# Performance work log

Hardware: AMD Instinct MI355X
Metric: run time of the kernel (lower is better)

## Reference

```python
import jax, jax.numpy as jnp
import numpy as np

H = 512  # hidden_size
A = 1.0  # hard_sigm slope


def hard_sigm(a, x):
    return jnp.clip((a * x + 1.0) / 2.0, 0.0, 1.0)


def setup_inputs() -> dict:
    key = jax.random.key(0)
    ks = jax.random.split(key, 10)
    B = 8192
    bottom, top = 512, 512
    stdv = 1.0 / np.sqrt(H)
    u = lambda k, shp: jax.random.uniform(k, shp, jnp.float32, -stdv, stdv)
    return {
        "c": jax.random.normal(ks[0], (H, B), jnp.float32),
        "h_bottom": jax.random.normal(ks[1], (bottom, B), jnp.float32),
        "h": jax.random.normal(ks[2], (H, B), jnp.float32),
        "h_top": jax.random.normal(ks[3], (top, B), jnp.float32),
        "z": jax.random.uniform(ks[4], (1, B), jnp.float32),
        "z_bottom": jax.random.uniform(ks[5], (1, B), jnp.float32),
        "U_11": u(ks[6], (4 * H + 1, H)),
        "U_21": u(ks[7], (4 * H + 1, top)),
        "W_01": u(ks[8], (4 * H + 1, bottom)),
        "bias": u(ks[9], (4 * H + 1,)),
    }


def reference(c, h_bottom, h, h_top, z, z_bottom, U_11, U_21, W_01, bias):
    # z, z_bottom: (1, B) boundary indicators broadcast over the gate axis
    s_recur = (1.0 - z) * (U_11 @ h)          # (4H+1, B)
    s_topdown = z * (U_21 @ h_top)            # last_layer=False
    s_bottomup = z_bottom * (W_01 @ h_bottom)
    f_s = s_recur + s_topdown + s_bottomup + bias[:, None]

    f = jax.nn.sigmoid(f_s[0:H, :])
    i = jax.nn.sigmoid(f_s[H:2 * H, :])
    o = jax.nn.sigmoid(f_s[2 * H:3 * H, :])
    g = jnp.tanh(f_s[3 * H:4 * H, :])
    z_hat = hard_sigm(A, f_s[4 * H:4 * H + 1, :])  # (1, B)

    ig = i * g
    c_new = z * ig + (1.0 - z) * (1.0 - z_bottom) * c \
        + (1.0 - z) * z_bottom * (f * c + ig)
    tanh_c = jnp.tanh(c_new)
    h_new = z * o * tanh_c + (1.0 - z) * (1.0 - z_bottom) * h \
        + (1.0 - z) * z_bottom * o * tanh_c
    return (h_new, c_new, z_hat)
```

## Files before the change

kernel.cpp:

```cpp
#include <hip/hip_runtime.h>
#include <hip/hip_bf16.h>

#define HH 512
#define BB 8192
#define KK 1536
#define NT 48
#define HB 4194304
#define BLOB 8192

typedef __bf16 bhalf;
typedef __bf16 bf16x8 __attribute__((ext_vector_type(8)));
typedef float  f32x4  __attribute__((ext_vector_type(4)));

typedef __attribute__((address_space(1))) void* as1_t;
typedef __attribute__((address_space(3))) void* as3_t;

#define GLDS(src, dst) __builtin_amdgcn_global_load_lds((as1_t)(void*)(src), (as3_t)(void*)(dst), 16, 0, 0)
#define SBAR() asm volatile("s_barrier" ::: "memory")
#define VM8()  asm volatile("s_waitcnt vmcnt(8)" ::: "memory")
#define VM4()  asm volatile("s_waitcnt vmcnt(4)" ::: "memory")
#define VM0()  asm volatile("s_waitcnt vmcnt(0)" ::: "memory")


__global__ __launch_bounds__(256) void prep_x(
    const float* __restrict__ h, const float* __restrict__ ht,
    const float* __restrict__ hb, const float* __restrict__ z,
    const float* __restrict__ zb, bhalf* __restrict__ XtP)
{
    __shared__ float tile[32][257];
    const int tid = threadIdx.x;
    const int kt  = blockIdx.x;
    const int nt  = blockIdx.y;
    const int n   = nt * 256 + tid;
    const int kb  = kt * 32;

    const float* src; int kr; float scale;
    if (kb < 512)       { src = h;  kr = kb;        scale = 1.f - z[n]; }
    else if (kb < 1024) { src = ht; kr = kb - 512;  scale = z[n]; }
    else                { src = hb; kr = kb - 1024; scale = zb[n]; }

    #pragma unroll
    for (int kk = 0; kk < 32; ++kk)
        tile[kk][tid] = src[(size_t)(kr + kk) * BB + n] * scale;
    __syncthreads();

    bhalf* blob = XtP + (size_t)(nt * NT + kt) * BLOB;
    #pragma unroll
    for (int q = 0; q < 4; ++q) {
        const int s  = q * 256 + tid;
        const int rb = s >> 6, w = s & 63;
        const int hh = w >> 4, lrr = w & 15;
        const int nloc = rb * 16 + lrr, kloc = hh * 8;
        bf16x8 r;
        #pragma unroll
        for (int e = 0; e < 8; ++e) r[e] = (bhalf)tile[kloc + e][nloc];
        *(bf16x8*)(blob + s * 8) = r;
    }
}

__global__ __launch_bounds__(256) void prep_w(
    const float* __restrict__ U11, const float* __restrict__ U21,
    const float* __restrict__ W01, bhalf* __restrict__ WcP)
{
    const int o    = blockIdx.x * 4 + (threadIdx.x >> 6);
    const int lane = threadIdx.x & 63;
    const int g = o >> 9, j = o & 511;
    const int mp = 4 * j + g;
    const int mt = mp >> 8, rb = (mp >> 4) & 15, lrr = mp & 15;

    #pragma unroll
    for (int p = 0; p < 3; ++p) {
        const float* src = (p == 0) ? U11 : (p == 1) ? U21 : W01;
        const float* rp  = src + (size_t)o * 512 + lane * 8;
        float4 v0 = *(const float4*)rp;
        float4 v1 = *(const float4*)(rp + 4);
        bf16x8 r;
        r[0]=(bhalf)v0.x; r[1]=(bhalf)v0.y; r[2]=(bhalf)v0.z; r[3]=(bhalf)v0.w;
        r[4]=(bhalf)v1.x; r[5]=(bhalf)v1.y; r[6]=(bhalf)v1.z; r[7]=(bhalf)v1.w;
        const int kt = p * 16 + (lane >> 2);
        const int hh = lane & 3;
        *(bf16x8*)(WcP + (size_t)(mt * NT + kt) * BLOB
                   + rb * 512 + hh * 128 + lrr * 8) = r;
    }
}

__device__ __forceinline__ float sigmf(float x)    { return 1.f / (1.f + __expf(-x)); }
__device__ __forceinline__ float tanhfast(float x) { return 2.f / (1.f + __expf(-2.f * x)) - 1.f; }

__device__ __forceinline__ void compute_tile(
    const bhalf* __restrict__ Ab, const bhalf* __restrict__ Bb,
    f32x4 (&acc)[8][4])
{
    bf16x8 bfr[4], afr[4];
    #pragma unroll
    for (int n = 0; n < 4; ++n) bfr[n] = *(const bf16x8*)(Bb + n * 512);
    #pragma unroll
    for (int m = 0; m < 4; ++m) afr[m] = *(const bf16x8*)(Ab + m * 512);
    __builtin_amdgcn_s_setprio(1);
    #pragma unroll
    for (int m = 0; m < 4; ++m)
        #pragma unroll
        for (int n = 0; n < 4; ++n)
            acc[m][n] = __builtin_amdgcn_mfma_f32_16x16x32_bf16(afr[m], bfr[n], acc[m][n], 0, 0, 0);
    __builtin_amdgcn_s_setprio(0);
    #pragma unroll
    for (int m = 0; m < 4; ++m) afr[m] = *(const bf16x8*)(Ab + (4 + m) * 512);
    __builtin_amdgcn_s_setprio(1);
    #pragma unroll
    for (int m = 0; m < 4; ++m)
        #pragma unroll
        for (int n = 0; n < 4; ++n)
            acc[4 + m][n] = __builtin_amdgcn_mfma_f32_16x16x32_bf16(afr[m], bfr[n], acc[4 + m][n], 0, 0, 0);
    __builtin_amdgcn_s_setprio(0);
}

__global__ __launch_bounds__(512, 2) void gemm_fused(
    const bhalf* __restrict__ WcP, const bhalf* __restrict__ XtP,
    const float* __restrict__ bias, const float* __restrict__ c_in,
    const float* __restrict__ h_in, const float* __restrict__ z,
    const float* __restrict__ zb, float* __restrict__ out)
{
    __shared__ bhalf As[4][BLOB];
    __shared__ bhalf Bs[4][BLOB];

    const int tid  = threadIdx.x;
    const int lane = tid & 63;
    const int wid  = tid >> 6;
    const int wm   = wid >> 2, wn = wid & 3;
    const int lr   = lane & 15, hi = lane >> 4;
    const int soff = hi * 128 + lr * 8;

    const int xcd = blockIdx.x & 7;
    const int i   = blockIdx.x >> 3;
    const int mt  = i & 7;
    const int nt  = xcd * 4 + (i >> 3);
    const int m0 = mt * 256, n0 = nt * 256;

    const bhalf* gA = WcP + (size_t)mt * (NT * BLOB) + tid * 8;
    const bhalf* gB = XtP + (size_t)nt * (NT * BLOB) + tid * 8;

#define STAGE(t) do {                                                   \
        const bhalf* sa_ = gA + (size_t)(t) * BLOB;                     \
        const bhalf* sb_ = gB + (size_t)(t) * BLOB;                     \
        bhalf* da_ = &As[(t) & 3][tid * 8];                             \
        bhalf* db_ = &Bs[(t) & 3][tid * 8];                             \
        GLDS(sa_, da_); GLDS(sa_ + 4096, da_ + 4096);                   \
        GLDS(sb_, db_); GLDS(sb_ + 4096, db_ + 4096);                   \
    } while (0)

    f32x4 acc[8][4] = {};

    STAGE(0); STAGE(1); STAGE(2);

    for (int tt = 0; tt < 44; tt += 4) {
        #pragma unroll
        for (int u = 0; u < 4; ++u) {
            VM8(); SBAR();
            STAGE(tt + u + 3);
            compute_tile(&As[u][wm * 4096 + soff], &Bs[u][wn * 2048 + soff], acc);
        }
    }
    VM8(); SBAR(); STAGE(47);
    compute_tile(&As[0][wm * 4096 + soff], &Bs[0][wn * 2048 + soff], acc);
    VM8(); SBAR();
    compute_tile(&As[1][wm * 4096 + soff], &Bs[1][wn * 2048 + soff], acc);
    VM4(); SBAR();
    compute_tile(&As[2][wm * 4096 + soff], &Bs[2][wn * 2048 + soff], acc);
    VM0(); SBAR();
    compute_tile(&As[3][wm * 4096 + soff], &Bs[3][wn * 2048 + soff], acc);

    const int colbase = n0 + wn * 64 + lr;
    float zc[4], zbc[4];
    #pragma unroll
    for (int ni = 0; ni < 4; ++ni) {
        zc[ni]  = z[colbase + ni * 16];
        zbc[ni] = zb[colbase + ni * 16];
    }
    #pragma unroll
    for (int mi = 0; mi < 8; ++mi) {
        const int j = (m0 >> 2) + wm * 32 + mi * 4 + hi;
        const float bf_ = bias[j];
        const float bi_ = bias[512 + j];
        const float bo_ = bias[1024 + j];
        const float bg_ = bias[1536 + j];
        #pragma unroll
        for (int ni = 0; ni < 4; ++ni) {
            const int col = colbase + ni * 16;
            const size_t idx = (size_t)j * BB + col;
            const float cv = c_in[idx];
            const float hv = h_in[idx];
            const float fv = sigmf(acc[mi][ni][0] + bf_);
            const float iv = sigmf(acc[mi][ni][1] + bi_);
            const float ov = sigmf(acc[mi][ni][2] + bo_);
            const float gv = tanhfast(acc[mi][ni][3] + bg_);
            const float ig = iv * gv;
            const float zq = zc[ni], zbq = zbc[ni];
            const float cn = zq * ig + (1.f - zq) * (1.f - zbq) * cv
                           + (1.f - zq) * zbq * (fv * cv + ig);
            const float tc = tanhfast(cn);
            const float hn = (zq + (1.f - zq) * zbq) * ov * tc
                           + (1.f - zq) * (1.f - zbq) * hv;
            out[idx]      = hn;
            out[HB + idx] = cn;
        }
    }
}

__global__ __launch_bounds__(256) void zhat_k(
    const bhalf* __restrict__ XtP, const float* __restrict__ U11,
    const float* __restrict__ U21, const float* __restrict__ W01,
    const float* __restrict__ bias, float* __restrict__ out)
{
    __shared__ float wlds[1536];
    __shared__ float red[8][32];
    const int tid = threadIdx.x;
    for (int idx = tid; idx < 1536; idx += 256) {
        float v;
        if (idx < 512)       v = U11[1048576 + idx];
        else if (idx < 1024) v = U21[1048576 + idx - 512];
        else                 v = W01[1048576 + idx - 1024];
        wlds[idx] = v;
    }
    __syncthreads();

    const int col = tid & 31, kg = tid >> 5;
    const int n = blockIdx.x * 32 + col;
    const int nt = n >> 8, rb = (n >> 4) & 15, lrr = n & 15;
    const bhalf* base = XtP + (size_t)nt * (NT * BLOB) + rb * 512;

    float acc = 0.f;
    for (int kt = kg * 6; kt < kg * 6 + 6; ++kt) {
        #pragma unroll
        for (int hh = 0; hh < 4; ++hh) {
            bf16x8 v = *(const bf16x8*)(base + (size_t)kt * BLOB + hh * 128 + lrr * 8);
            #pragma unroll
            for (int e = 0; e < 8; ++e)
                acc += (float)v[e] * wlds[kt * 32 + hh * 8 + e];
        }
    }
    red[kg][col] = acc;
    __syncthreads();
    if (tid < 32) {
        float s = 0.f;
        #pragma unroll
        for (int k2 = 0; k2 < 8; ++k2) s += red[k2][tid];
        const float v = (s + bias[2048] + 1.f) * 0.5f;
        out[(size_t)2 * HB + blockIdx.x * 32 + tid] = fminf(fmaxf(v, 0.f), 1.f);
    }
}

extern "C" void kernel_launch(void* const* d_in, const int* in_sizes, int n_in,
                              void* d_out, int out_size, void* d_ws, size_t ws_size,
                              hipStream_t stream) {
    const float* c    = (const float*)d_in[0];
    const float* hb   = (const float*)d_in[1];
    const float* h    = (const float*)d_in[2];
    const float* ht   = (const float*)d_in[3];
    const float* z    = (const float*)d_in[4];
    const float* zb   = (const float*)d_in[5];
    const float* U11  = (const float*)d_in[6];
    const float* U21  = (const float*)d_in[7];
    const float* W01  = (const float*)d_in[8];
    const float* bias = (const float*)d_in[9];
    float* out = (float*)d_out;

    char* ws = (char*)d_ws;
    bhalf* XtP = (bhalf*)ws;
    bhalf* WcP = (bhalf*)(ws + 25165824);

    prep_x    <<<dim3(48, 32), 256, 0, stream>>>(h, ht, hb, z, zb, XtP);
    prep_w    <<<512, 256, 0, stream>>>(U11, U21, W01, WcP);
    gemm_fused<<<256, 512, 0, stream>>>(WcP, XtP, bias, c, h, z, zb, out);
    zhat_k    <<<256, 256, 0, stream>>>(XtP, U11, U21, W01, bias, out);
}
```

Baseline: 81.79 us.

## Restructure GEMM main loop into split-phase LDS-read/MFMA pipeline with register double-buffering

Replaces the per-tile compute_tile call with a two-phase schedule per K-tile. The high A fragments are read while the low half's MFMAs run, and the next tile's B and low A fragments are prefetched into a second register set during the high half. Global-to-LDS staging is split into separate A and B issues spread across the phases, with finer vmcnt waits and extra barriers around each MFMA cluster. The aim is to hide LDS read latency behind MFMAs and smooth memory issue. It adds barriers and register pressure, which could lower occupancy under launch_bounds(512,2).

```diff
diff --git a/kernel.cpp b/kernel.cpp
--- a/kernel.cpp
+++ b/kernel.cpp
@@ -18,6 +18,7 @@
 #define GLDS(src, dst) __builtin_amdgcn_global_load_lds((as1_t)(void*)(src), (as3_t)(void*)(dst), 16, 0, 0)
 #define SBAR() asm volatile("s_barrier" ::: "memory")
 #define VM8()  asm volatile("s_waitcnt vmcnt(8)" ::: "memory")
+#define VM6()  asm volatile("s_waitcnt vmcnt(6)" ::: "memory")
 #define VM4()  asm volatile("s_waitcnt vmcnt(4)" ::: "memory")
 #define VM0()  asm volatile("s_waitcnt vmcnt(0)" ::: "memory")
 
@@ -87,33 +88,6 @@
 __device__ __forceinline__ float sigmf(float x)    { return 1.f / (1.f + __expf(-x)); }
 __device__ __forceinline__ float tanhfast(float x) { return 2.f / (1.f + __expf(-2.f * x)) - 1.f; }
 
-__device__ __forceinline__ void compute_tile(
-    const bhalf* __restrict__ Ab, const bhalf* __restrict__ Bb,
-    f32x4 (&acc)[8][4])
-{
-    bf16x8 bfr[4], afr[4];
-    #pragma unroll
-    for (int n = 0; n < 4; ++n) bfr[n] = *(const bf16x8*)(Bb + n * 512);
-    #pragma unroll
-    for (int m = 0; m < 4; ++m) afr[m] = *(const bf16x8*)(Ab + m * 512);
-    __builtin_amdgcn_s_setprio(1);
-    #pragma unroll
-    for (int m = 0; m < 4; ++m)
-        #pragma unroll
-        for (int n = 0; n < 4; ++n)
-            acc[m][n] = __builtin_amdgcn_mfma_f32_16x16x32_bf16(afr[m], bfr[n], acc[m][n], 0, 0, 0);
-    __builtin_amdgcn_s_setprio(0);
-    #pragma unroll
-    for (int m = 0; m < 4; ++m) afr[m] = *(const bf16x8*)(Ab + (4 + m) * 512);
-    __builtin_amdgcn_s_setprio(1);
-    #pragma unroll
-    for (int m = 0; m < 4; ++m)
-        #pragma unroll
-        for (int n = 0; n < 4; ++n)
-            acc[4 + m][n] = __builtin_amdgcn_mfma_f32_16x16x32_bf16(afr[m], bfr[n], acc[4 + m][n], 0, 0, 0);
-    __builtin_amdgcn_s_setprio(0);
-}
-
 __global__ __launch_bounds__(512, 2) void gemm_fused(
     const bhalf* __restrict__ WcP, const bhalf* __restrict__ XtP,
     const float* __restrict__ bias, const float* __restrict__ c_in,
@@ -139,35 +113,87 @@
     const bhalf* gA = WcP + (size_t)mt * (NT * BLOB) + tid * 8;
     const bhalf* gB = XtP + (size_t)nt * (NT * BLOB) + tid * 8;
 
-#define STAGE(t) do {                                                   \
-        const bhalf* sa_ = gA + (size_t)(t) * BLOB;                     \
-        const bhalf* sb_ = gB + (size_t)(t) * BLOB;                     \
-        bhalf* da_ = &As[(t) & 3][tid * 8];                             \
-        bhalf* db_ = &Bs[(t) & 3][tid * 8];                             \
-        GLDS(sa_, da_); GLDS(sa_ + 4096, da_ + 4096);                   \
-        GLDS(sb_, db_); GLDS(sb_ + 4096, db_ + 4096);                   \
-    } while (0)
+    const bhalf* pA0 = &As[0][wm * 4096 + soff];
+    const bhalf* pA1 = &As[1][wm * 4096 + soff];
+    const bhalf* pA2 = &As[2][wm * 4096 + soff];
+    const bhalf* pA3 = &As[3][wm * 4096 + soff];
+    const bhalf* pB0 = &Bs[0][wn * 2048 + soff];
+    const bhalf* pB1 = &Bs[1][wn * 2048 + soff];
+    const bhalf* pB2 = &Bs[2][wn * 2048 + soff];
+    const bhalf* pB3 = &Bs[3][wn * 2048 + soff];
+
+#define STAGE_A(t, bf) do { const bhalf* s_ = gA + (size_t)(t) * BLOB;        \
+        GLDS(s_, &As[bf][tid * 8]); GLDS(s_ + 4096, &As[bf][tid * 8 + 4096]); } while (0)
+#define STAGE_B(t, bf) do { const bhalf* s_ = gB + (size_t)(t) * BLOB;        \
+        GLDS(s_, &Bs[bf][tid * 8]); GLDS(s_ + 4096, &Bs[bf][tid * 8 + 4096]); } while (0)
+
+#define RDA(bf, i_) (*(const bf16x8*)(pA##bf + (i_) * 512))
+#define RDB(bf, i_) (*(const bf16x8*)(pB##bf + (i_) * 512))
+
+#define MF(mi, ni, A_, B_) acc[mi][ni] = \
+    __builtin_amdgcn_mfma_f32_16x16x32_bf16(A_, B_, acc[mi][ni], 0, 0, 0)
+
+#define CL_LO(B0,B1,B2,B3) do { __builtin_amdgcn_s_setprio(1);                \
+    MF(0,0,aL0,B0); MF(0,1,aL0,B1); MF(0,2,aL0,B2); MF(0,3,aL0,B3);           \
+    MF(1,0,aL1,B0); MF(1,1,aL1,B1); MF(1,2,aL1,B2); MF(1,3,aL1,B3);           \
+    MF(2,0,aL2,B0); MF(2,1,aL2,B1); MF(2,2,aL2,B2); MF(2,3,aL2,B3);           \
+    MF(3,0,aL3,B0); MF(3,1,aL3,B1); MF(3,2,aL3,B2); MF(3,3,aL3,B3);           \
+    __builtin_amdgcn_s_setprio(0); } while (0)
+
+#define CL_HI(B0,B1,B2,B3) do { __builtin_amdgcn_s_setprio(1);                \
+    MF(4,0,aH0,B0); MF(4,1,aH0,B1); MF(4,2,aH0,B2); MF(4,3,aH0,B3);           \
+    MF(5,0,aH1,B0); MF(5,1,aH1,B1); MF(5,2,aH1,B2); MF(5,3,aH1,B3);           \
+    MF(6,0,aH2,B0); MF(6,1,aH2,B1); MF(6,2,aH2,B2); MF(6,3,aH2,B3);           \
+    MF(7,0,aH3,B0); MF(7,1,aH3,B1); MF(7,2,aH3,B2); MF(7,3,aH3,B3);           \
+    __builtin_amdgcn_s_setprio(0); } while (0)
+
+#define PH0(bfc, tst, bfst, DOST, B0,B1,B2,B3) do {                           \
+    aH0 = RDA(bfc,4); aH1 = RDA(bfc,5); aH2 = RDA(bfc,6); aH3 = RDA(bfc,7);   \
+    if (DOST) STAGE_A(tst, bfst);                                             \
+    SBAR(); CL_LO(B0,B1,B2,B3); SBAR(); } while (0)
+
+#define PH1(bfn, tst, bfst, DOST, DORD, VMW, B0,B1,B2,B3, N0,N1,N2,N3) do {   \
+    VMW;                                                                      \
+    if (DORD) { N0 = RDB(bfn,0); N1 = RDB(bfn,1); N2 = RDB(bfn,2);            \
+                N3 = RDB(bfn,3);                                              \
+                aL0 = RDA(bfn,0); aL1 = RDA(bfn,1); aL2 = RDA(bfn,2);         \
+                aL3 = RDA(bfn,3); }                                           \
+    if (DOST) STAGE_B(tst, bfst);                                             \
+    SBAR(); CL_HI(B0,B1,B2,B3); SBAR(); } while (0)
 
     f32x4 acc[8][4] = {};
-
-    STAGE(0); STAGE(1); STAGE(2);
-
-    for (int tt = 0; tt < 44; tt += 4) {
-        #pragma unroll
-        for (int u = 0; u < 4; ++u) {
-            VM8(); SBAR();
-            STAGE(tt + u + 3);
-            compute_tile(&As[u][wm * 4096 + soff], &Bs[u][wn * 2048 + soff], acc);
-        }
-    }
-    VM8(); SBAR(); STAGE(47);
-    compute_tile(&As[0][wm * 4096 + soff], &Bs[0][wn * 2048 + soff], acc);
+    bf16x8 aL0, aL1, aL2, aL3, aH0, aH1, aH2, aH3;
+    bf16x8 bA0, bA1, bA2, bA3, bB0, bB1, bB2, bB3;
+
+    STAGE_A(0, 0); STAGE_B(0, 0);
+    STAGE_A(1, 1); STAGE_B(1, 1);
+    STAGE_A(2, 2); STAGE_B(2, 2);
     VM8(); SBAR();
-    compute_tile(&As[1][wm * 4096 + soff], &Bs[1][wn * 2048 + soff], acc);
-    VM4(); SBAR();
-    compute_tile(&As[2][wm * 4096 + soff], &Bs[2][wn * 2048 + soff], acc);
-    VM0(); SBAR();
-    compute_tile(&As[3][wm * 4096 + soff], &Bs[3][wn * 2048 + soff], acc);
+    bA0 = RDB(0,0); bA1 = RDB(0,1); bA2 = RDB(0,2); bA3 = RDB(0,3);
+    aL0 = RDA(0,0); aL1 = RDA(0,1); aL2 = RDA(0,2); aL3 = RDA(0,3);
+
+#define QUAD(base) do {                                                       \
+    PH0(0, (base)+3, 3, 1, bA0,bA1,bA2,bA3);                                  \
+    PH1(1, (base)+3, 3, 1, 1, VM6(), bA0,bA1,bA2,bA3, bB0,bB1,bB2,bB3);       \
+    PH0(1, (base)+4, 0, 1, bB0,bB1,bB2,bB3);                                  \
+    PH1(2, (base)+4, 0, 1, 1, VM6(), bB0,bB1,bB2,bB3, bA0,bA1,bA2,bA3);       \
+    PH0(2, (base)+5, 1, 1, bA0,bA1,bA2,bA3);                                  \
+    PH1(3, (base)+5, 1, 1, 1, VM6(), bA0,bA1,bA2,bA3, bB0,bB1,bB2,bB3);       \
+    PH0(3, (base)+6, 2, 1, bB0,bB1,bB2,bB3);                                  \
+    PH1(0, (base)+6, 2, 1, 1, VM6(), bB0,bB1,bB2,bB3, bA0,bA1,bA2,bA3);       \
+} while (0)
+
+    for (int base = 0; base < 44; base += 4) {
+        QUAD(base);
+    }
+    PH0(0, 47, 3, 1, bA0,bA1,bA2,bA3);
+    PH1(1, 47, 3, 1, 1, VM6(), bA0,bA1,bA2,bA3, bB0,bB1,bB2,bB3);
+    PH0(1, 0, 0, 0, bB0,bB1,bB2,bB3);
+    PH1(2, 0, 0, 0, 1, VM4(), bB0,bB1,bB2,bB3, bA0,bA1,bA2,bA3);
+    PH0(2, 0, 0, 0, bA0,bA1,bA2,bA3);
+    PH1(3, 0, 0, 0, 1, VM0(), bA0,bA1,bA2,bA3, bB0,bB1,bB2,bB3);
+    PH0(3, 0, 0, 0, bB0,bB1,bB2,bB3);
+    PH1(0, 0, 0, 0, 0, ((void)0), bB0,bB1,bB2,bB3, bA0,bA1,bA2,bA3);
 
     const int colbase = n0 + wn * 64 + lr;
     float zc[4], zbc[4];
```

After: 85.37 us. 1.04x slower.
